# Performance work log

Hardware: AMD Instinct MI355X
Metric: run time of the kernel (lower is better)

Reference implementation:

```python
import jax, jax.numpy as jnp
import numpy as np

B, L, D = 4, 2048, 256
EXPAND, D_STATE, D_CONV = 2, 16, 4
D_INNER = EXPAND * D
DT_RANK = (D + 15) // 16  # ceil(d_model/16) = 16
N_HEADS = 4
H_MLP = int(D * 4.0)
EPS = 1e-5


def _ln(x, w, b):
    mu = x.mean(-1, keepdims=True)
    var = ((x - mu) ** 2).mean(-1, keepdims=True)
    return (x - mu) / jnp.sqrt(var + EPS) * w + b


def _silu(x):
    return x * jax.nn.sigmoid(x)


def _mamba(x, Win, convw, convb, Wx, Wdt, bdt, Alog, Dp, Wout):
    # x: (B, L, D) -> (B, L, D). Standard Mamba mixer (selective scan).
    b, l, d = x.shape
    xz = x @ Win.T                      # (b, l, 2*d_inner)
    xi, z = jnp.split(xz, 2, axis=-1)
    # depthwise causal conv1d, kernel D_CONV
    xc = jnp.swapaxes(xi, 1, 2)         # (b, d_inner, l)
    xc = jax.lax.conv_general_dilated(
        xc, convw, (1,), [(D_CONV - 1, 0)],
        feature_group_count=D_INNER, dimension_numbers=('NCW', 'OIW', 'NCW'))
    xi = _silu(jnp.swapaxes(xc + convb[None, :, None], 1, 2))  # (b, l, d_inner)
    dbl = xi @ Wx.T                     # (b, l, dt_rank + 2*d_state)
    dt = jax.nn.softplus(dbl[..., :DT_RANK] @ Wdt.T + bdt)     # (b, l, d_inner)
    Bm = dbl[..., DT_RANK:DT_RANK + D_STATE]                    # (b, l, n)
    Cm = dbl[..., DT_RANK + D_STATE:]                            # (b, l, n)
    A = -jnp.exp(Alog)                  # (d_inner, n)

    def step(h, ins):
        dt_t, B_t, C_t, u_t = ins       # (b,d_inner),(b,n),(b,n),(b,d_inner)
        h = h * jnp.exp(dt_t[..., None] * A) + dt_t[..., None] * B_t[:, None, :] * u_t[..., None]
        return h, jnp.einsum('bdn,bn->bd', h, C_t)

    xs = tuple(jnp.swapaxes(t, 0, 1) for t in (dt, Bm, Cm, xi))  # time-major
    h0 = jnp.zeros((b, D_INNER, D_STATE), x.dtype)
    _, ys = jax.lax.scan(step, h0, xs)  # ys: (l, b, d_inner)
    y = jnp.swapaxes(ys, 0, 1) + xi * Dp
    return (y * _silu(z)) @ Wout.T


def _attn(x, Wqkv, bqkv, Wo, bo):
    b, l, d = x.shape
    hd = d // N_HEADS
    qkv = x @ Wqkv.T + bqkv
    q, k, v = jnp.split(qkv, 3, axis=-1)
    sh = lambda t: t.reshape(b, l, N_HEADS, hd).transpose(0, 2, 1, 3)
    q, k, v = sh(q), sh(k), sh(v)
    a = jax.nn.softmax(jnp.einsum('bhqd,bhkd->bhqk', q, k) / np.float32(np.sqrt(hd)), axis=-1)
    o = jnp.einsum('bhqk,bhkd->bhqd', a, v).transpose(0, 2, 1, 3).reshape(b, l, d)
    return o @ Wo.T + bo


def setup_inputs() -> dict:
    key = jax.random.key(0)
    ks = iter(jax.random.split(key, 40))
    rn = lambda shape, s=0.02: jax.random.normal(next(ks), shape, jnp.float32) * s
    inp = {'x': jax.random.normal(next(ks), (B, L, D), jnp.float32)}
    for p in ('mf', 'mb'):
        inp[p + '_Win'] = rn((2 * D_INNER, D))
        inp[p + '_convw'] = rn((D_INNER, 1, D_CONV), 0.1)
        inp[p + '_convb'] = jnp.zeros((D_INNER,), jnp.float32)
        inp[p + '_Wx'] = rn((DT_RANK + 2 * D_STATE, D_INNER))
        inp[p + '_Wdt'] = rn((D_INNER, DT_RANK), 0.1)
        inp[p + '_bdt'] = rn((D_INNER,), 0.5)
        inp[p + '_Alog'] = jnp.log(jnp.broadcast_to(jnp.arange(1, D_STATE + 1, dtype=jnp.float32), (D_INNER, D_STATE)))
        inp[p + '_D'] = jnp.ones((D_INNER,), jnp.float32)
        inp[p + '_Wout'] = rn((D, D_INNER))
    for n in ('n1', 'n2', 'n3'):
        inp[n + 'w'] = jnp.ones((D,), jnp.float32)
        inp[n + 'b'] = jnp.zeros((D,), jnp.float32)
    inp['Wqkv'] = rn((3 * D, D))
    inp['bqkv'] = jnp.zeros((3 * D,), jnp.float32)
    inp['Wo'] = rn((D, D))
    inp['bo'] = jnp.zeros((D,), jnp.float32)
    inp['fc1w'] = rn((H_MLP, D))
    inp['fc1b'] = jnp.zeros((H_MLP,), jnp.float32)
    inp['fc2w'] = rn((D, H_MLP))
    inp['fc2b'] = jnp.zeros((D,), jnp.float32)
    return inp


def reference(x, n1w, n1b, n2w, n2b, n3w, n3b,
              mf_Win, mf_convw, mf_convb, mf_Wx, mf_Wdt, mf_bdt, mf_Alog, mf_D, mf_Wout,
              mb_Win, mb_convw, mb_convb, mb_Wx, mb_Wdt, mb_bdt, mb_Alog, mb_D, mb_Wout,
              Wqkv, bqkv, Wo, bo, fc1w, fc1b, fc2w, fc2b):
    # Mamba branch (bidirectional): DropPath is identity at eval
    h = _ln(x, n1w, n1b)
    fwd = _mamba(h, mf_Win, mf_convw, mf_convb, mf_Wx, mf_Wdt, mf_bdt, mf_Alog, mf_D, mf_Wout)
    bwd = jnp.flip(_mamba(jnp.flip(h, 1), mb_Win, mb_convw, mb_convb, mb_Wx, mb_Wdt, mb_bdt, mb_Alog, mb_D, mb_Wout), 1)
    x = x + fwd + bwd
    # Attention branch (full attention since window=None)
    x = x + _attn(_ln(x, n2w, n2b), Wqkv, bqkv, Wo, bo)
    # MLP branch (exact GELU like torch default)
    h = _ln(x, n3w, n3b)
    x = x + (jax.nn.gelu(h @ fc1w.T + fc1b, approximate=False) @ fc2w.T + fc2b)
    return x
```

## Files before the change

### kernel.cpp

```cpp
#include <hip/hip_runtime.h>
#include <hip/hip_bf16.h>
#include <math.h>

#define LL 2048
#define DD 256
#define MTOT 8192
#define DINNER 512
#define CT 32
#define NC 64

typedef __attribute__((ext_vector_type(8))) short short8;
typedef __attribute__((ext_vector_type(4))) float f32x4;

__device__ __forceinline__ float us2f(unsigned short u){
  return __uint_as_float(((unsigned)u) << 16);
}
__device__ __forceinline__ unsigned short f2us(float f){
  __hip_bfloat16 h = __float2bfloat16(f);
  return *(unsigned short*)&h;
}
__device__ __forceinline__ float frcp(float x){
  return __builtin_amdgcn_rcpf(x);
}

__global__ void probe_kernel(const unsigned* __restrict__ alog, int* __restrict__ flag){
  if (threadIdx.x == 0 && blockIdx.x == 0) *flag = (alog[0] != 0u) ? 1 : 0;
}

struct Srcs { const void* p[32]; unsigned off[33]; unsigned foff[32]; };

__global__ __launch_bounds__(256) void cvt_all_kernel(Srcs s, float* __restrict__ dst,
                                                      unsigned short* __restrict__ db,
                                                      const int* __restrict__ flag,
                                                      unsigned total){
  unsigned i = blockIdx.x * 256u + threadIdx.x;
  if (i >= total) return;
  int k = 31;
  while (s.off[k] > i) --k;
  unsigned j = i - s.off[k];
  float v;
  if (*flag) v = us2f(((const unsigned short*)s.p[k])[j]);
  else       v = ((const float*)s.p[k])[j];
  if ((k == 24 && j < 65536u) || (k == 25 && j < 256u)) v *= 0.125f;
  db[i] = f2us(v);
  if (s.foff[k] != 0xFFFFFFFFu) dst[s.foff[k] + j] = v;
}

__global__ __launch_bounds__(256) void cvt_x_kernel(const void* __restrict__ src,
                                                    float* __restrict__ dst,
                                                    const int* __restrict__ flag, unsigned n){
  unsigned i = blockIdx.x * 256u + threadIdx.x;
  if (i >= n) return;
  if (*flag) dst[i] = us2f(((const unsigned short*)src)[i]);
  else       dst[i] = ((const float*)src)[i];
}

__global__ __launch_bounds__(256) void wdbl_prep_kernel(
    const float* __restrict__ Wx, int dsWx, unsigned short* __restrict__ Wd)
{
  const unsigned g = blockIdx.x * 256u + threadIdx.x;
  const int dir = g >> 15;
  const unsigned idx = g & 32767u;
  const int n = idx >> 9, k = idx & 511;
  float v = (n < 48) ? (Wx + (size_t)dir * dsWx)[(size_t)n * 512 + k] : 0.f;
  Wd[g] = f2us(v);
}

__global__ __launch_bounds__(256) void final_out_kernel(
    const float* __restrict__ xf, void* __restrict__ out,
    const int* __restrict__ flag, unsigned n)
{
  unsigned i = blockIdx.x * 256u + threadIdx.x;
  if (i >= n) return;
  float v = xf[i];
  if (*flag) ((unsigned short*)out)[i] = f2us(v);
  else       ((float*)out)[i] = v;
}

enum { G_BF16=0, G_GELU=1, G_RESID=2, G_STF=3 };
__global__ __launch_bounds__(256) void gemm_mfma_kernel(
    const unsigned short* __restrict__ A, int lda, int agap,
    const unsigned short* __restrict__ W, const unsigned short* __restrict__ W2,
    int Kw, int nsplit, int ksplit, int msplit,
    const float* __restrict__ bias,
    unsigned short* __restrict__ Cb, float* __restrict__ resid,
    int N, int K, int kslices, int mode)
{
  __shared__ unsigned short sA[64][40];
  __shared__ unsigned short sW[64][40];
  const int tid = threadIdx.x;
  const int w = tid >> 6, lane = tid & 63, quad = lane >> 4, l16 = lane & 15;
  const int m0 = blockIdx.y << 6, n0 = blockIdx.x << 6;
  const int ks = blockIdx.z;
  const int kper = K / kslices;
  const int srow = tid >> 2, skc = (tid & 3) << 3;
  int wr = n0 + srow;
  const unsigned short* Wbase = W;
  if (msplit && m0 >= msplit) Wbase = W2;
  if (nsplit && wr >= nsplit){ Wbase = W2; wr -= nsplit; }
  f32x4 acc[4] = {};
  for (int k0 = ks * kper; k0 < ks * kper + kper; k0 += 32){
    int ac = k0 + skc;
    if (agap && ac >= 512) ac += 512;
    short8 av = *(const short8*)(A + (size_t)(m0 + srow) * lda + ac);
    int kk = k0 + skc;
    const unsigned short* Wp = Wbase;
    if (ksplit && kk >= ksplit){ Wp = W2; kk -= ksplit; }
    short8 wv = *(const short8*)(Wp + (size_t)wr * Kw + kk);
    __syncthreads();
    *(short8*)&sA[srow][skc] = av;
    *(short8*)&sW[srow][skc] = wv;
    __syncthreads();
    short8 af = *(const short8*)&sA[w * 16 + l16][quad << 3];
    #pragma unroll
    for (int ns = 0; ns < 4; ++ns){
      short8 wf = *(const short8*)&sW[ns * 16 + l16][quad << 3];
      acc[ns] = __builtin_amdgcn_mfma_f32_16x16x32_bf16(af, wf, acc[ns], 0, 0, 0);
    }
  }
  #pragma unroll
  for (int ns = 0; ns < 4; ++ns){
    const int n = n0 + ns * 16 + l16;
    const float bv = (bias && ks == 0) ? bias[n] : 0.f;
    #pragma unroll
    for (int r = 0; r < 4; ++r){
      const int m = m0 + w * 16 + quad * 4 + r;
      const size_t off = (size_t)m * N + n;
      float v = acc[ns][r] + bv;
      if (mode == G_BF16) Cb[off] = f2us(v);
      else if (mode == G_GELU) Cb[off] = f2us(0.5f * v * (1.f + erff(v * 0.70710678118f)));
      else if (mode == G_RESID) resid[off] += v;
      else resid[off] = v;
    }
  }
}

__global__ __launch_bounds__(256) void gemm128_kernel(
    const unsigned short* __restrict__ A, int lda,
    const unsigned short* __restrict__ W, const unsigned short* __restrict__ W2,
    int Kw, int nsplit, const float* __restrict__ bias,
    unsigned short* __restrict__ Cb, int N, int K, int mode)
{
  __shared__ unsigned short sA[128][40];
  __shared__ unsigned short sW[128][40];
  const int tid = threadIdx.x;
  const int w = tid >> 6, lane = tid & 63, quad = lane >> 4, l16 = lane & 15;
  const int wm = (w >> 1) << 6, wn = (w & 1) << 6;
  const int m0 = blockIdx.y << 7, n0 = blockIdx.x << 7;
  const int srow = tid >> 2, skc = (tid & 3) << 3;
  const unsigned short* wrp0;
  const unsigned short* wrp1;
  {
    int r0 = n0 + srow, r1 = n0 + srow + 64;
    const unsigned short* b0 = W;
    const unsigned short* b1 = W;
    if (nsplit){
      if (r0 >= nsplit){ b0 = W2; r0 -= nsplit; }
      if (r1 >= nsplit){ b1 = W2; r1 -= nsplit; }
    }
    wrp0 = b0 + (size_t)r0 * Kw;
    wrp1 = b1 + (size_t)r1 * Kw;
  }
  const unsigned short* arp0 = A + (size_t)(m0 + srow) * lda;
  const unsigned short* arp1 = A + (size_t)(m0 + srow + 64) * lda;
  f32x4 acc[4][4] = {};
  for (int k0 = 0; k0 < K; k0 += 32){
    short8 av0 = *(const short8*)(arp0 + k0 + skc);
    short8 av1 = *(const short8*)(arp1 + k0 + skc);
    short8 wv0 = *(const short8*)(wrp0 + k0 + skc);
    short8 wv1 = *(const short8*)(wrp1 + k0 + skc);
    __syncthreads();
    *(short8*)&sA[srow][skc] = av0;
    *(short8*)&sA[srow + 64][skc] = av1;
    *(short8*)&sW[srow][skc] = wv0;
    *(short8*)&sW[srow + 64][skc] = wv1;
    __syncthreads();
    short8 af[4], wf[4];
    #pragma unroll
    for (int i = 0; i < 4; ++i){
      af[i] = *(const short8*)&sA[wm + i * 16 + l16][quad << 3];
      wf[i] = *(const short8*)&sW[wn + i * 16 + l16][quad << 3];
    }
    #pragma unroll
    for (int mi = 0; mi < 4; ++mi)
      #pragma unroll
      for (int ni = 0; ni < 4; ++ni)
        acc[mi][ni] = __builtin_amdgcn_mfma_f32_16x16x32_bf16(af[mi], wf[ni], acc[mi][ni], 0, 0, 0);
  }
  #pragma unroll
  for (int ni = 0; ni < 4; ++ni){
    const int n = n0 + wn + ni * 16 + l16;
    const float bv = bias ? bias[n] : 0.f;
    #pragma unroll
    for (int mi = 0; mi < 4; ++mi){
      #pragma unroll
      for (int r = 0; r < 4; ++r){
        const int m = m0 + wm + mi * 16 + quad * 4 + r;
        float v = acc[mi][ni][r] + bv;
        if (mode == G_GELU) v = 0.5f * v * (1.f + erff(v * 0.70710678118f));
        Cb[(size_t)m * N + n] = f2us(v);
      }
    }
  }
}

__global__ __launch_bounds__(256) void ln_kernel(
    const float* __restrict__ xin,
    const float* __restrict__ w, const float* __restrict__ b,
    unsigned short* __restrict__ hout)
{
  const int row = blockIdx.x, tid = threadIdx.x;
  const size_t off = (size_t)row * DD + tid;
  float v = xin[off];
  float s = v, s2 = v * v;
  #pragma unroll
  for (int o = 32; o; o >>= 1){ s += __shfl_xor(s, o); s2 += __shfl_xor(s2, o); }
  __shared__ float ls[4], ls2[4];
  if ((tid & 63) == 0){ ls[tid >> 6] = s; ls2[tid >> 6] = s2; }
  __syncthreads();
  s  = ls[0] + ls[1] + ls[2] + ls[3];
  s2 = ls2[0] + ls2[1] + ls2[2] + ls2[3];
  const float mu  = s * (1.f / DD);
  const float var = s2 * (1.f / DD) - mu * mu;
  const float inv = rsqrtf(var + 1e-5f);
  hout[off] = f2us((v - mu) * inv * w[tid] + b[tid]);
}

__global__ __launch_bounds__(256) void conv_silu_kernel(
    const unsigned short* __restrict__ xzc, const float* __restrict__ convw0, int dsCw,
    const float* __restrict__ convb0, int dsCb, unsigned short* __restrict__ xi)
{
  const unsigned g = blockIdx.x * 256u + threadIdx.x;
  const int c4 = (g & 127) << 2;
  const int t = (g >> 7) & 2047;
  const int b = (g >> 18) & 3;
  const int dir = g >> 20;
  const float* cw = convw0 + (size_t)dir * dsCw;
  float4 acc = *(const float4*)(convb0 + (size_t)dir * dsCb + c4);
  float wv[4][4];
  #pragma unroll
  for (int j = 0; j < 4; ++j) *(float4*)wv[j] = *(const float4*)(cw + (c4 + j) * 4);
  #pragma unroll
  for (int k = 0; k < 4; ++k){
    const int tt = dir ? (t + (3 - k)) : (t - 3 + k);
    if ((unsigned)tt < 2048u){
      ushort4 x = *(const ushort4*)(xzc + ((size_t)(b * 2048 + tt)) * 2048 + dir * 1024 + c4);
      acc.x = fmaf(wv[0][k], us2f(x.x), acc.x);
      acc.y = fmaf(wv[1][k], us2f(x.y), acc.y);
      acc.z = fmaf(wv[2][k], us2f(x.z), acc.z);
      acc.w = fmaf(wv[3][k], us2f(x.w), acc.w);
    }
  }
  ushort4 o;
  o.x = f2us(acc.x * frcp(1.f + __expf(-acc.x)));
  o.y = f2us(acc.y * frcp(1.f + __expf(-acc.y)));
  o.z = f2us(acc.z * frcp(1.f + __expf(-acc.z)));
  o.w = f2us(acc.w * frcp(1.f + __expf(-acc.w)));
  *(ushort4*)(xi + (size_t)dir * 4194304 + ((size_t)(b * 2048 + t)) * 512 + c4) = o;
}

__global__ __launch_bounds__(256) void scan_part1_kernel(
    const unsigned short* __restrict__ xib, int dsXi,
    const float* __restrict__ dblc,
    const float* __restrict__ Alog, int dsAl,
    const float* __restrict__ Wdt0, int dsWdt,
    const float* __restrict__ bdt0, int dsBdt,
    float* __restrict__ dtsum, int dsDts,
    float* __restrict__ hend, int dsHend)
{
  const int bx = blockIdx.x;
  const int dg = bx & 1, c = (bx >> 1) & (NC - 1), b = (bx >> 7) & 3, dir = bx >> 9;
  const int tid = threadIdx.x;
  const int d = dg * 256 + tid;
  const unsigned short* xi_ = xib + (size_t)dir * dsXi;
  const float* Al_ = Alog + (size_t)dir * dsAl;
  __shared__ float sDB[CT][32];
  __shared__ unsigned short sXI[CT][256];
  {
    const int s = tid >> 3, c4 = (tid & 7) << 2;
    const int t = dir ? (LL - 1 - (c * CT + s)) : (c * CT + s);
    *(float4*)&sDB[s][c4] =
      *(const float4*)(dblc + ((size_t)(dir * 8192 + b * LL + t)) * 64 + c4);
  }
  #pragma unroll
  for (int p = 0; p < 4; ++p){
    const int s = p * 8 + (tid >> 5);
    const int dc = (tid & 31) << 3;
    const int t = dir ? (LL - 1 - (c * CT + s)) : (c * CT + s);
    *(short8*)&sXI[s][dc] =
      *(const short8*)(xi_ + ((size_t)(b * LL + t)) * 512 + dg * 256 + dc);
  }
  float wdt[16];
  {
    const float* wr = Wdt0 + (size_t)dir * dsWdt + (size_t)d * 16;
    #pragma unroll
    for (int q = 0; q < 4; ++q) *(float4*)&wdt[q * 4] = *(const float4*)(wr + q * 4);
  }
  const float bdtd = (bdt0 + (size_t)dir * dsBdt)[d];
  float A[16];
  #pragma unroll
  for (int n = 0; n < 16; ++n) A[n] = -__expf(Al_[d * 16 + n]);
  const float A1 = A[0];
  bool fast = true;
  #pragma unroll
  for (int n = 0; n < 16; ++n)
    fast = fast && (fabsf(A[n] - A1 * (n + 1)) <= 1e-4f * fabsf(A1 * (n + 1)) + 1e-30f);
  __syncthreads();
  float h[16];
  #pragma unroll
  for (int n = 0; n < 16; ++n) h[n] = 0.f;
  float dts = 0.f;
  #pragma unroll 1
  for (int s = 0; s < CT; ++s){
    const float uv = us2f(sXI[s][tid]);
    f32x4 dv[4], Bv[4];
    #pragma unroll
    for (int q = 0; q < 4; ++q) dv[q] = *(const f32x4*)&sDB[s][q * 4];
    #pragma unroll
    for (int q = 0; q < 4; ++q) Bv[q] = *(const f32x4*)&sDB[s][16 + q * 4];
    float p0 = 0.f, p1 = 0.f, p2 = 0.f, p3 = 0.f;
    #pragma unroll
    for (int j = 0; j < 4; ++j){
      p0 = fmaf(dv[0][j], wdt[j],      p0);
      p1 = fmaf(dv[1][j], wdt[4 + j],  p1);
      p2 = fmaf(dv[2][j], wdt[8 + j],  p2);
      p3 = fmaf(dv[3][j], wdt[12 + j], p3);
    }
    const float dtpre = bdtd + ((p0 + p1) + (p2 + p3));
    const float dtv = (dtpre > 20.f) ? dtpre : __logf(1.f + __expf(dtpre));
    const float dtu = dtv * uv;
    dts += dtv;
    if (fast){
      const float e1 = __expf(dtv * A1);
      const float e2 = e1 * e1;
      float eo = e1, ev = e2;
      #pragma unroll
      for (int m = 0; m < 8; ++m){
        h[2 * m]     = fmaf(h[2 * m],     eo, dtu * Bv[(2 * m) >> 2][(2 * m) & 3]);
        h[2 * m + 1] = fmaf(h[2 * m + 1], ev, dtu * Bv[(2 * m + 1) >> 2][(2 * m + 1) & 3]);
        eo *= e2; ev *= e2;
      }
    } else {
      #pragma unroll
      for (int n = 0; n < 16; ++n){
        const float e = __expf(dtv * A[n]);
        h[n] = fmaf(h[n], e, dtu * Bv[n >> 2][n & 3]);
      }
    }
  }
  const size_t base = (size_t)dir * dsHend + ((size_t)((b * NC + c) * 512 + d)) * 16;
  #pragma unroll
  for (int q = 0; q < 4; ++q) *(float4*)&hend[base + q * 4] = *(const float4*)&h[q * 4];
  dtsum[(size_t)dir * dsDts + (size_t)(b * NC + c) * 512 + d] = dts;
}

__global__ __launch_bounds__(256) void scan_combine_kernel(
    const float* __restrict__ dtsum, int dsDts,
    float* __restrict__ hend, int dsHend,
    const float* __restrict__ Alog, int dsAl)
{
  const unsigned g = blockIdx.x * 256u + threadIdx.x;
  const int dir = g >> 15;
  const unsigned gg = g & 32767u;
  const int b = gg >> 13, d = (gg >> 4) & 511, n = gg & 15;
  const float A = -__expf((Alog + (size_t)dir * dsAl)[d * 16 + n]);
  const float* dts_ = dtsum + (size_t)dir * dsDts;
  float* he_ = hend + (size_t)dir * dsHend;
  float h = 0.f;
  for (int c = 0; c < NC; ++c){
    const size_t sb = ((size_t)((b * NC + c) * 512 + d)) * 16 + n;
    const float e = __expf(dts_[(size_t)(b * NC + c) * 512 + d] * A);
    const float he = he_[sb];
    he_[sb] = h;
    h = h * e + he;
  }
}

__global__ __launch_bounds__(256) void scan_part2_kernel(
    const unsigned short* __restrict__ xib, int dsXi,
    const float* __restrict__ dblc,
    const unsigned short* __restrict__ zin,
    unsigned short* __restrict__ yout,
    const float* __restrict__ Alog, int dsAl,
    const float* __restrict__ Wdt0, int dsWdt,
    const float* __restrict__ bdt0, int dsBdt,
    const float* __restrict__ Dp, int dsD,
    const float* __restrict__ hin, int dsHend)
{
  const int bx = blockIdx.x;
  const int dg = bx & 1, c = (bx >> 1) & (NC - 1), b = (bx >> 7) & 3, dir = bx >> 9;
  const int tid = threadIdx.x;
  const int d = dg * 256 + tid;
  const unsigned short* xi_ = xib + (size_t)dir * dsXi;
  const unsigned short* z_ = zin + dir * 1024;
  unsigned short* y_ = yout + dir * 1024;
  const float* Al_ = Alog + (size_t)dir * dsAl;
  __shared__ float sDB[CT][48];
  __shared__ unsigned short sXI[CT][256];
  __shared__ unsigned short sZ[CT][256];
  for (int i4 = tid; i4 < 384; i4 += 256){
    const int s = i4 / 12, cc = (i4 - s * 12) << 2;
    const int t = dir ? (LL - 1 - (c * CT + s)) : (c * CT + s);
    *(float4*)&sDB[s][cc] =
      *(const float4*)(dblc + ((size_t)(dir * 8192 + b * LL + t)) * 64 + cc);
  }
  #pragma unroll
  for (int p = 0; p < 4; ++p){
    const int s = p * 8 + (tid >> 5);
    const int dc = (tid & 31) << 3;
    const int t = dir ? (LL - 1 - (c * CT + s)) : (c * CT + s);
    const size_t row = (size_t)(b * LL + t);
    *(short8*)&sXI[s][dc] = *(const short8*)(xi_ + row * 512 + dg * 256 + dc);
    *(short8*)&sZ[s][dc]  = *(const short8*)(z_ + row * 2048 + dg * 256 + dc);
  }
  float wdt[16];
  {
    const float* wr = Wdt0 + (size_t)dir * dsWdt + (size_t)d * 16;
    #pragma unroll
    for (int q = 0; q < 4; ++q) *(float4*)&wdt[q * 4] = *(const float4*)(wr + q * 4);
  }
  const float bdtd = (bdt0 + (size_t)dir * dsBdt)[d];
  float A[16];
  #pragma unroll
  for (int n = 0; n < 16; ++n) A[n] = -__expf(Al_[d * 16 + n]);
  const float A1 = A[0];
  bool fast = true;
  #pragma unroll
  for (int n = 0; n < 16; ++n)
    fast = fast && (fabsf(A[n] - A1 * (n + 1)) <= 1e-4f * fabsf(A1 * (n + 1)) + 1e-30f);
  const float Dv = (Dp + (size_t)dir * dsD)[d];
  __syncthreads();
  float h[16];
  const size_t base = (size_t)dir * dsHend + ((size_t)((b * NC + c) * 512 + d)) * 16;
  #pragma unroll
  for (int q = 0; q < 4; ++q) *(float4*)&h[q * 4] = *(const float4*)&hin[base + q * 4];
  #pragma unroll 1
  for (int s = 0; s < CT; ++s){
    const int t = dir ? (LL - 1 - (c * CT + s)) : (c * CT + s);
    const size_t row = (size_t)(b * LL + t);
    const float uv = us2f(sXI[s][tid]);
    const float z  = us2f(sZ[s][tid]);
    f32x4 dv[4];
    #pragma unroll
    for (int q = 0; q < 4; ++q) dv[q] = *(const f32x4*)&sDB[s][q * 4];
    float p0 = 0.f, p1 = 0.f, p2 = 0.f, p3 = 0.f;
    #pragma unroll
    for (int j = 0; j < 4; ++j){
      p0 = fmaf(dv[0][j], wdt[j],      p0);
      p1 = fmaf(dv[1][j], wdt[4 + j],  p1);
      p2 = fmaf(dv[2][j], wdt[8 + j],  p2);
      p3 = fmaf(dv[3][j], wdt[12 + j], p3);
    }
    const float dtpre = bdtd + ((p0 + p1) + (p2 + p3));
    const float dtv = (dtpre > 20.f) ? dtpre : __logf(1.f + __expf(dtpre));
    const float dtu = dtv * uv;
    f32x4 Bv[4], Cv[4];
    #pragma unroll
    for (int q = 0; q < 4; ++q) Bv[q] = *(const f32x4*)&sDB[s][16 + q * 4];
    #pragma unroll
    for (int q = 0; q < 4; ++q) Cv[q] = *(const f32x4*)&sDB[s][32 + q * 4];
    float pA = uv * Dv, pB = 0.f;
    if (fast){
      const float e1 = __expf(dtv * A1);
      const float e2 = e1 * e1;
      float eo = e1, ev = e2;
      #pragma unroll
      for (int m = 0; m < 8; ++m){
        const int n0 = 2 * m, n1 = 2 * m + 1;
        h[n0] = fmaf(h[n0], eo, dtu * Bv[n0 >> 2][n0 & 3]);
        pA = fmaf(h[n0], Cv[n0 >> 2][n0 & 3], pA);
        h[n1] = fmaf(h[n1], ev, dtu * Bv[n1 >> 2][n1 & 3]);
        pB = fmaf(h[n1], Cv[n1 >> 2][n1 & 3], pB);
        eo *= e2; ev *= e2;
      }
    } else {
      #pragma unroll
      for (int n = 0; n < 16; ++n){
        const float e = __expf(dtv * A[n]);
        h[n] = fmaf(h[n], e, dtu * Bv[n >> 2][n & 3]);
        pA = fmaf(h[n], Cv[n >> 2][n & 3], pA);
      }
    }
    const float p = pA + pB;
    const float sig = frcp(1.f + __expf(-z));
    y_[row * 2048 + d] = f2us(p * z * sig);
  }
}

__global__ __launch_bounds__(256) void v_prep_kernel(
    const unsigned short* __restrict__ qkvb, unsigned short* __restrict__ Vt)
{
  const int kt = blockIdx.x;
  const int bh = blockIdx.y;
  const int b = bh >> 2, h = bh & 3;
  __shared__ unsigned short tile[64][72];
  #pragma unroll
  for (int rr = 0; rr < 4; ++rr){
    const int idx = (rr * 256 + threadIdx.x) * 4;
    const int key = idx >> 6, d = idx & 63;
    ushort4 v = *(const ushort4*)(qkvb + ((size_t)(b * 2048 + kt * 64 + key)) * 768 + 512 + h * 64 + d);
    *(ushort4*)&tile[key][d] = v;
  }
  __syncthreads();
  #pragma unroll
  for (int rr = 0; rr < 8; ++rr){
    const int o2 = rr * 256 + threadIdx.x;
    const int d = o2 >> 5, k2 = (o2 & 31) << 1;
    ushort2 u;
    u.x = tile[k2][d];
    u.y = tile[k2 + 1][d];
    *(ushort2*)(Vt + (size_t)bh * 131072 + (size_t)d * 2048 + kt * 64 + k2) = u;
  }
}

__global__ __launch_bounds__(256) void attn_mfma_kernel(
    const unsigned short* __restrict__ qkvb, const unsigned short* __restrict__ Vt,
    float* __restrict__ op0, float* __restrict__ op1, float* __restrict__ lpart)
{
  __shared__ unsigned short sK[64][72];
  __shared__ unsigned short sV[64][72];
  __shared__ unsigned short sP[4][32][68];
  const int tid = threadIdx.x;
  const int w = tid >> 6, lane = tid & 63, quad = lane >> 4, l16 = lane & 15;
  const int bh = blockIdx.y;
  const int b = bh >> 2, h = bh & 3;
  const int q0 = blockIdx.x * 128;
  const int split = blockIdx.z;

  short8 qf[2][2];
  #pragma unroll
  for (int qs = 0; qs < 2; ++qs){
    const unsigned short* qp = qkvb + ((size_t)(b * 2048 + q0 + w * 32 + qs * 16 + l16)) * 768 + h * 64 + quad * 8;
    qf[qs][0] = *(const short8*)qp;
    qf[qs][1] = *(const short8*)(qp + 32);
  }

  f32x4 o[2][4] = {};
  float lsum[2][4] = {};

  const int kt0 = split * 512;
  for (int kt = kt0; kt < kt0 + 512; kt += 64){
    __syncthreads();
    #pragma unroll
    for (int r = 0; r < 2; ++r){
      const int idx = (r * 256 + tid) * 8;
      const int row = idx >> 6, c = idx & 63;
      *(short8*)&sK[row][c] = *(const short8*)(qkvb + ((size_t)(b * 2048 + kt + row)) * 768 + 256 + h * 64 + c);
      *(short8*)&sV[row][c] = *(const short8*)(Vt + (size_t)bh * 131072 + (size_t)row * 2048 + kt + c);
    }
    __syncthreads();

    #pragma unroll
    for (int qs = 0; qs < 2; ++qs){
      float p[4][4];
      #pragma unroll
      for (int sub = 0; sub < 4; ++sub){
        short8 bk0 = *(const short8*)&sK[sub * 16 + l16][quad * 8];
        short8 bk1 = *(const short8*)&sK[sub * 16 + l16][32 + quad * 8];
        f32x4 acc = {0,0,0,0};
        acc = __builtin_amdgcn_mfma_f32_16x16x32_bf16(qf[qs][0], bk0, acc, 0, 0, 0);
        acc = __builtin_amdgcn_mfma_f32_16x16x32_bf16(qf[qs][1], bk1, acc, 0, 0, 0);
        #pragma unroll
        for (int r = 0; r < 4; ++r) p[sub][r] = __expf(acc[r]);
      }
      #pragma unroll
      for (int r = 0; r < 4; ++r)
        lsum[qs][r] += p[0][r] + p[1][r] + p[2][r] + p[3][r];
      #pragma unroll
      for (int sub = 0; sub < 4; ++sub)
        #pragma unroll
        for (int r = 0; r < 4; ++r)
          sP[w][qs * 16 + quad * 4 + r][sub * 16 + l16] = f2us(p[sub][r]);
    }
    __builtin_amdgcn_s_waitcnt(0);
    #pragma unroll
    for (int qs = 0; qs < 2; ++qs){
      short8 pa0 = *(const short8*)&sP[w][qs * 16 + l16][quad * 8];
      short8 pa1 = *(const short8*)&sP[w][qs * 16 + l16][32 + quad * 8];
      #pragma unroll
      for (int nsub = 0; nsub < 4; ++nsub){
        short8 bv0 = *(const short8*)&sV[nsub * 16 + l16][quad * 8];
        short8 bv1 = *(const short8*)&sV[nsub * 16 + l16][32 + quad * 8];
        o[qs][nsub] = __builtin_amdgcn_mfma_f32_16x16x32_bf16(pa0, bv0, o[qs][nsub], 0, 0, 0);
        o[qs][nsub] = __builtin_amdgcn_mfma_f32_16x16x32_bf16(pa1, bv1, o[qs][nsub], 0, 0, 0);
      }
    }
  }

  float* op = (split < 2 ? op0 : op1) + (size_t)(split & 1) * 2097152;
  #pragma unroll
  for (int qs = 0; qs < 2; ++qs){
    #pragma unroll
    for (int r = 0; r < 4; ++r){
      float l = lsum[qs][r];
      l += __shfl_xor(l, 1); l += __shfl_xor(l, 2);
      l += __shfl_xor(l, 4); l += __shfl_xor(l, 8);
      const int q = q0 + w * 32 + qs * 16 + quad * 4 + r;
      #pragma unroll
      for (int nsub = 0; nsub < 4; ++nsub)
        op[((size_t)bh * 2048 + q) * 64 + nsub * 16 + l16] = o[qs][nsub][r];
      if (l16 == 0) lpart[(split * 16 + bh) * 2048 + q] = l;
    }
  }
}

__global__ __launch_bounds__(256) void attn_merge_kernel(
    const float* __restrict__ op0, const float* __restrict__ op1,
    const float* __restrict__ lpart, unsigned short* __restrict__ outp)
{
  const unsigned g = blockIdx.x * 256u + threadIdx.x;
  const int d4 = (g & 15) << 2;
  const int q = (g >> 4) & 2047;
  const int bh = g >> 15;
  float4 s = make_float4(0.f, 0.f, 0.f, 0.f);
  float l = 0.f;
  #pragma unroll
  for (int sp = 0; sp < 4; ++sp){
    const float* op = (sp < 2 ? op0 : op1) + (size_t)(sp & 1) * 2097152;
    float4 o = *(const float4*)(op + ((size_t)bh * 2048 + q) * 64 + d4);
    s.x += o.x; s.y += o.y; s.z += o.z; s.w += o.w;
    l += lpart[(sp * 16 + bh) * 2048 + q];
  }
  const float invl = 1.f / l;
  const int b = bh >> 2, h = bh & 3;
  ushort4 u;
  u.x = f2us(s.x * invl);
  u.y = f2us(s.y * invl);
  u.z = f2us(s.z * invl);
  u.w = f2us(s.w * invl);
  *(ushort4*)(outp + ((size_t)(b * 2048 + q)) * 256 + h * 64 + d4) = u;
}

extern "C" void kernel_launch(void* const* d_in, const int* in_sizes, int n_in,
                              void* d_out, int out_size, void* d_ws, size_t ws_size,
                              hipStream_t stream)
{
  static const bool needf[33] = {
    false, false,true,true,true,true,true,true,true,false,
    false,true,true,true,true,true,true,true,false,
    true,true,true,true,true,true,
    false,true,false,true,false,true,false,true };

  int* flag  = (int*)d_ws;
  float* wts = (float*)d_ws + 16;

  Srcs srcs;
  unsigned acc = 0, facc = 0;
  unsigned foff_h[33];
  for (int i = 1; i <= 32; ++i){
    srcs.p[i - 1] = d_in[i];
    srcs.off[i - 1] = acc;
    acc += (unsigned)in_sizes[i];
    if (needf[i]){ srcs.foff[i - 1] = facc; foff_h[i] = facc; facc += (unsigned)in_sizes[i]; }
    else { srcs.foff[i - 1] = 0xFFFFFFFFu; foff_h[i] = 0xFFFFFFFFu; }
  }
  srcs.off[32] = acc;
  const unsigned wtotal = acc;
  const unsigned ftot = (facc + 3u) & ~3u;

  unsigned short* wb16 = (unsigned short*)(wts + ftot);
  float* xf    = wts + ftot + (wtotal + 1) / 2;
  float* xzc_f = xf + 2097152;
  float* xi_f  = xzc_f + 8388608;
  float* dblc  = xi_f + 4194304;
  float* hb_f  = dblc + 1048576;
  float* hend  = hb_f + 1048576;
  float* dtsum = hend + 4194304;
  float* wd_f  = dtsum + 262144;

  unsigned short* xzc  = (unsigned short*)xzc_f;
  unsigned short* xi16 = (unsigned short*)xi_f;
  unsigned short* hb16 = (unsigned short*)hb_f;
  unsigned short* wdbl = (unsigned short*)wd_f;
  unsigned short* qkvb = xzc;
  unsigned short* Vt   = (unsigned short*)hend;
  float* op0   = xzc_f + 4194304;
  float* op1   = xi_f;
  float* lpart = dtsum;
  unsigned short* fc1o = xzc;

  auto wp  = [&](int i){ return wts + foff_h[i]; };
  auto wp16= [&](int i){ return wb16 + srcs.off[i - 1]; };

  hipLaunchKernelGGL(probe_kernel, dim3(1), dim3(64), 0, stream,
      (const unsigned*)d_in[7], flag);
  hipLaunchKernelGGL(cvt_all_kernel, dim3((wtotal + 255) / 256), dim3(256), 0, stream,
      srcs, wts, wb16, flag, wtotal);
  hipLaunchKernelGGL(cvt_x_kernel, dim3(MTOT * DD / 256), dim3(256), 0, stream,
      d_in[0], xf, flag, (unsigned)(MTOT * DD));

  const int dsCw = (int)(foff_h[11] - foff_h[2]);
  const int dsAl = (int)(foff_h[16] - foff_h[7]);
  const int dsD  = (int)(foff_h[17] - foff_h[8]);
  const int dsWx = (int)(foff_h[13] - foff_h[4]);
  const int dsWdt= (int)(foff_h[14] - foff_h[5]);
  const int dsBdt= (int)(foff_h[15] - foff_h[6]);
  const int dsCb2= (int)(foff_h[12] - foff_h[3]);

  hipLaunchKernelGGL(wdbl_prep_kernel, dim3(256), dim3(256), 0, stream,
      wp(4), dsWx, wdbl);

  auto gemm16 = [&](const unsigned short* Ab, int lda, int agap, int M,
                    const unsigned short* W, const unsigned short* W2,
                    int Kw, int nsplit, int ksplit, int msplit, const float* bias,
                    unsigned short* Cb, float* resid,
                    int N, int K, int ksl, int mode){
    hipLaunchKernelGGL(gemm_mfma_kernel, dim3(N / 64, M / 64, ksl), dim3(256), 0, stream,
        Ab, lda, agap, W, W2, Kw, nsplit, ksplit, msplit, bias, Cb, resid, N, K, ksl, mode);
  };
  auto gemm128 = [&](const unsigned short* Ab, int lda, int M,
                     const unsigned short* W, const unsigned short* W2,
                     int Kw, int nsplit, const float* bias,
                     unsigned short* Cb, int N, int K, int mode){
    hipLaunchKernelGGL(gemm128_kernel, dim3(N / 128, M / 128), dim3(256), 0, stream,
        Ab, lda, W, W2, Kw, nsplit, bias, Cb, N, K, mode);
  };

  hipLaunchKernelGGL(ln_kernel, dim3(MTOT), dim3(256), 0, stream,
      xf, wp(19), wp(20), hb16);

  gemm128(hb16, 256, MTOT, wp16(1), wp16(10), 256, 1024, nullptr,
          xzc, 2048, 256, G_BF16);
  hipLaunchKernelGGL(conv_silu_kernel, dim3(8192), dim3(256), 0, stream,
      xzc, wp(2), dsCw, wp(3), dsCb2, xi16);
  gemm16(xi16, 512, 0, 2 * MTOT, wdbl, wdbl + 32768, 512, 0, 0, MTOT, nullptr,
         nullptr, dblc, 64, 512, 1, G_STF);
  hipLaunchKernelGGL(scan_part1_kernel, dim3(1024), dim3(256), 0, stream,
      xi16, 4194304, dblc, wp(7), dsAl, wp(5), dsWdt, wp(6), dsBdt,
      dtsum, 131072, hend, 2097152);
  hipLaunchKernelGGL(scan_combine_kernel, dim3(256), dim3(256), 0, stream,
      dtsum, 131072, hend, 2097152, wp(7), dsAl);
  hipLaunchKernelGGL(scan_part2_kernel, dim3(1024), dim3(256), 0, stream,
      xi16, 4194304, dblc, xzc + 512, xzc, wp(7), dsAl, wp(5), dsWdt, wp(6), dsBdt,
      wp(8), dsD, hend, 2097152);
  gemm16(xzc, 2048, 1, MTOT, wp16(9), wp16(18), 512, 0, 512, 0, nullptr,
         nullptr, xf, 256, 1024, 1, G_RESID);

  hipLaunchKernelGGL(ln_kernel, dim3(MTOT), dim3(256), 0, stream,
      xf, wp(21), wp(22), hb16);
  gemm128(hb16, 256, MTOT, wp16(25), nullptr, 256, 0, wp(26),
          qkvb, 768, 256, G_BF16);
  hipLaunchKernelGGL(v_prep_kernel, dim3(32, 16), dim3(256), 0, stream,
      qkvb, Vt);
  hipLaunchKernelGGL(attn_mfma_kernel, dim3(16, 16, 4), dim3(256), 0, stream,
      qkvb, Vt, op0, op1, lpart);
  hipLaunchKernelGGL(attn_merge_kernel, dim3(2048), dim3(256), 0, stream,
      op0, op1, lpart, hb16);
  gemm16(hb16, 256, 0, MTOT, wp16(27), nullptr, 256, 0, 0, 0, wp(28),
         nullptr, xf, 256, 256, 1, G_RESID);

  hipLaunchKernelGGL(ln_kernel, dim3(MTOT), dim3(256), 0, stream,
      xf, wp(23), wp(24), hb16);
  gemm128(hb16, 256, MTOT, wp16(29), nullptr, 256, 0, wp(30),
          fc1o, 1024, 256, G_GELU);
  gemm16(fc1o, 1024, 0, MTOT, wp16(31), nullptr, 1024, 0, 0, 0, nullptr,
         nullptr, xf, 256, 1024, 1, G_RESID);
  hipLaunchKernelGGL(final_out_kernel, dim3(MTOT * DD / 256), dim3(256), 0, stream,
      xf, d_out, flag, (unsigned)(MTOT * DD));
}
```

Measured before the change: 439.9 us.

## Fuse input/output conversion, parallelize scan combine, drop attention split-K merge

Folds the input dtype conversion into the first layernorm and the final output conversion into the last GEMM epilogue, removing two elementwise kernels. Replaces the serial per-chunk scan combine loop with a wavefront-parallel prefix scan over chunks using shuffles, launched with many more blocks. Restructures attention to process 64 queries per block over the full key range, normalizing in-kernel, which removes the split-K partial buffers and the merge kernel at the cost of fewer, longer-running blocks.

```diff
diff --git a/kernel.cpp b/kernel.cpp
--- a/kernel.cpp
+++ b/kernel.cpp
@@ -46,15 +46,6 @@
   if (s.foff[k] != 0xFFFFFFFFu) dst[s.foff[k] + j] = v;
 }
 
-__global__ __launch_bounds__(256) void cvt_x_kernel(const void* __restrict__ src,
-                                                    float* __restrict__ dst,
-                                                    const int* __restrict__ flag, unsigned n){
-  unsigned i = blockIdx.x * 256u + threadIdx.x;
-  if (i >= n) return;
-  if (*flag) dst[i] = us2f(((const unsigned short*)src)[i]);
-  else       dst[i] = ((const float*)src)[i];
-}
-
 __global__ __launch_bounds__(256) void wdbl_prep_kernel(
     const float* __restrict__ Wx, int dsWx, unsigned short* __restrict__ Wd)
 {
@@ -66,25 +57,15 @@
   Wd[g] = f2us(v);
 }
 
-__global__ __launch_bounds__(256) void final_out_kernel(
-    const float* __restrict__ xf, void* __restrict__ out,
-    const int* __restrict__ flag, unsigned n)
-{
-  unsigned i = blockIdx.x * 256u + threadIdx.x;
-  if (i >= n) return;
-  float v = xf[i];
-  if (*flag) ((unsigned short*)out)[i] = f2us(v);
-  else       ((float*)out)[i] = v;
-}
-
-enum { G_BF16=0, G_GELU=1, G_RESID=2, G_STF=3 };
+enum { G_BF16=0, G_GELU=1, G_RESID=2, G_STF=3, G_OUT=4 };
 __global__ __launch_bounds__(256) void gemm_mfma_kernel(
     const unsigned short* __restrict__ A, int lda, int agap,
     const unsigned short* __restrict__ W, const unsigned short* __restrict__ W2,
     int Kw, int nsplit, int ksplit, int msplit,
     const float* __restrict__ bias,
     unsigned short* __restrict__ Cb, float* __restrict__ resid,
-    int N, int K, int kslices, int mode)
+    int N, int K, int kslices, int mode,
+    const int* __restrict__ flag, void* __restrict__ outp)
 {
   __shared__ unsigned short sA[64][40];
   __shared__ unsigned short sW[64][40];
@@ -94,6 +75,7 @@
   const int ks = blockIdx.z;
   const int kper = K / kslices;
   const int srow = tid >> 2, skc = (tid & 3) << 3;
+  const int fl = flag ? *flag : 0;
   int wr = n0 + srow;
   const unsigned short* Wbase = W;
   if (msplit && m0 >= msplit) Wbase = W2;
@@ -130,7 +112,12 @@
       if (mode == G_BF16) Cb[off] = f2us(v);
       else if (mode == G_GELU) Cb[off] = f2us(0.5f * v * (1.f + erff(v * 0.70710678118f)));
       else if (mode == G_RESID) resid[off] += v;
-      else resid[off] = v;
+      else if (mode == G_STF) resid[off] = v;
+      else {
+        const float t = v + resid[off];
+        if (fl) ((unsigned short*)outp)[off] = f2us(t);
+        else    ((float*)outp)[off] = t;
+      }
     }
   }
 }
@@ -212,6 +199,32 @@
   const int row = blockIdx.x, tid = threadIdx.x;
   const size_t off = (size_t)row * DD + tid;
   float v = xin[off];
+  float s = v, s2 = v * v;
+  #pragma unroll
+  for (int o = 32; o; o >>= 1){ s += __shfl_xor(s, o); s2 += __shfl_xor(s2, o); }
+  __shared__ float ls[4], ls2[4];
+  if ((tid & 63) == 0){ ls[tid >> 6] = s; ls2[tid >> 6] = s2; }
+  __syncthreads();
+  s  = ls[0] + ls[1] + ls[2] + ls[3];
+  s2 = ls2[0] + ls2[1] + ls2[2] + ls2[3];
+  const float mu  = s * (1.f / DD);
+  const float var = s2 * (1.f / DD) - mu * mu;
+  const float inv = rsqrtf(var + 1e-5f);
+  hout[off] = f2us((v - mu) * inv * w[tid] + b[tid]);
+}
+
+__global__ __launch_bounds__(256) void ln_first_kernel(
+    const void* __restrict__ src, const int* __restrict__ flag,
+    float* __restrict__ xf,
+    const float* __restrict__ w, const float* __restrict__ b,
+    unsigned short* __restrict__ hout)
+{
+  const int row = blockIdx.x, tid = threadIdx.x;
+  const size_t off = (size_t)row * DD + tid;
+  float v;
+  if (*flag) v = us2f(((const unsigned short*)src)[off]);
+  else       v = ((const float*)src)[off];
+  xf[off] = v;
   float s = v, s2 = v * v;
   #pragma unroll
   for (int o = 32; o; o >>= 1){ s += __shfl_xor(s, o); s2 += __shfl_xor(s2, o); }
@@ -359,21 +372,26 @@
     float* __restrict__ hend, int dsHend,
     const float* __restrict__ Alog, int dsAl)
 {
-  const unsigned g = blockIdx.x * 256u + threadIdx.x;
-  const int dir = g >> 15;
-  const unsigned gg = g & 32767u;
-  const int b = gg >> 13, d = (gg >> 4) & 511, n = gg & 15;
+  const int tid = threadIdx.x;
+  const int lane = tid & 63;
+  const unsigned gw = blockIdx.x * 4u + (tid >> 6);
+  const int n = gw & 15, d = (gw >> 4) & 511, b = (gw >> 13) & 3, dir = gw >> 15;
   const float A = -__expf((Alog + (size_t)dir * dsAl)[d * 16 + n]);
   const float* dts_ = dtsum + (size_t)dir * dsDts;
   float* he_ = hend + (size_t)dir * dsHend;
-  float h = 0.f;
-  for (int c = 0; c < NC; ++c){
-    const size_t sb = ((size_t)((b * NC + c) * 512 + d)) * 16 + n;
-    const float e = __expf(dts_[(size_t)(b * NC + c) * 512 + d] * A);
-    const float he = he_[sb];
-    he_[sb] = h;
-    h = h * e + he;
-  }
+  const int c = lane;
+  const size_t sb = ((size_t)((b * NC + c) * 512 + d)) * 16 + n;
+  float E = __expf(dts_[(size_t)(b * NC + c) * 512 + d] * A);
+  float H = he_[sb];
+  #pragma unroll
+  for (int off = 1; off < 64; off <<= 1){
+    const float Eu = __shfl_up(E, off);
+    const float Hu = __shfl_up(H, off);
+    if (lane >= off){ H = fmaf(Hu, E, H); E = Eu * E; }
+  }
+  float hin = __shfl_up(H, 1);
+  if (lane == 0) hin = 0.f;
+  he_[sb] = hin;
 }
 
 __global__ __launch_bounds__(256) void scan_part2_kernel(
@@ -515,31 +533,28 @@
 
 __global__ __launch_bounds__(256) void attn_mfma_kernel(
     const unsigned short* __restrict__ qkvb, const unsigned short* __restrict__ Vt,
-    float* __restrict__ op0, float* __restrict__ op1, float* __restrict__ lpart)
+    unsigned short* __restrict__ outp)
 {
   __shared__ unsigned short sK[64][72];
   __shared__ unsigned short sV[64][72];
-  __shared__ unsigned short sP[4][32][68];
+  __shared__ unsigned short sP[4][16][68];
   const int tid = threadIdx.x;
   const int w = tid >> 6, lane = tid & 63, quad = lane >> 4, l16 = lane & 15;
   const int bh = blockIdx.y;
   const int b = bh >> 2, h = bh & 3;
-  const int q0 = blockIdx.x * 128;
-  const int split = blockIdx.z;
-
-  short8 qf[2][2];
-  #pragma unroll
-  for (int qs = 0; qs < 2; ++qs){
-    const unsigned short* qp = qkvb + ((size_t)(b * 2048 + q0 + w * 32 + qs * 16 + l16)) * 768 + h * 64 + quad * 8;
-    qf[qs][0] = *(const short8*)qp;
-    qf[qs][1] = *(const short8*)(qp + 32);
-  }
-
-  f32x4 o[2][4] = {};
-  float lsum[2][4] = {};
-
-  const int kt0 = split * 512;
-  for (int kt = kt0; kt < kt0 + 512; kt += 64){
+  const int q0 = blockIdx.x * 64;
+
+  short8 qf[2];
+  {
+    const unsigned short* qp = qkvb + ((size_t)(b * 2048 + q0 + w * 16 + l16)) * 768 + h * 64 + quad * 8;
+    qf[0] = *(const short8*)qp;
+    qf[1] = *(const short8*)(qp + 32);
+  }
+
+  f32x4 o[4] = {};
+  float lsum[4] = {};
+
+  for (int kt = 0; kt < 2048; kt += 64){
     __syncthreads();
     #pragma unroll
     for (int r = 0; r < 2; ++r){
@@ -550,85 +565,49 @@
     }
     __syncthreads();
 
-    #pragma unroll
-    for (int qs = 0; qs < 2; ++qs){
-      float p[4][4];
+    float p[4][4];
+    #pragma unroll
+    for (int sub = 0; sub < 4; ++sub){
+      short8 bk0 = *(const short8*)&sK[sub * 16 + l16][quad * 8];
+      short8 bk1 = *(const short8*)&sK[sub * 16 + l16][32 + quad * 8];
+      f32x4 acc = {0,0,0,0};
+      acc = __builtin_amdgcn_mfma_f32_16x16x32_bf16(qf[0], bk0, acc, 0, 0, 0);
+      acc = __builtin_amdgcn_mfma_f32_16x16x32_bf16(qf[1], bk1, acc, 0, 0, 0);
       #pragma unroll
-      for (int sub = 0; sub < 4; ++sub){
-        short8 bk0 = *(const short8*)&sK[sub * 16 + l16][quad * 8];
-        short8 bk1 = *(const short8*)&sK[sub * 16 + l16][32 + quad * 8];
-        f32x4 acc = {0,0,0,0};
-        acc = __builtin_amdgcn_mfma_f32_16x16x32_bf16(qf[qs][0], bk0, acc, 0, 0, 0);
-        acc = __builtin_amdgcn_mfma_f32_16x16x32_bf16(qf[qs][1], bk1, acc, 0, 0, 0);
-        #pragma unroll
-        for (int r = 0; r < 4; ++r) p[sub][r] = __expf(acc[r]);
-      }
+      for (int r = 0; r < 4; ++r) p[sub][r] = __expf(acc[r]);
+    }
+    #pragma unroll
+    for (int r = 0; r < 4; ++r)
+      lsum[r] += p[0][r] + p[1][r] + p[2][r] + p[3][r];
+    #pragma unroll
+    for (int sub = 0; sub < 4; ++sub)
       #pragma unroll
       for (int r = 0; r < 4; ++r)
-        lsum[qs][r] += p[0][r] + p[1][r] + p[2][r] + p[3][r];
-      #pragma unroll
-      for (int sub = 0; sub < 4; ++sub)
-        #pragma unroll
-        for (int r = 0; r < 4; ++r)
-          sP[w][qs * 16 + quad * 4 + r][sub * 16 + l16] = f2us(p[sub][r]);
-    }
+        sP[w][quad * 4 + r][sub * 16 + l16] = f2us(p[sub][r]);
     __builtin_amdgcn_s_waitcnt(0);
-    #pragma unroll
-    for (int qs = 0; qs < 2; ++qs){
-      short8 pa0 = *(const short8*)&sP[w][qs * 16 + l16][quad * 8];
-      short8 pa1 = *(const short8*)&sP[w][qs * 16 + l16][32 + quad * 8];
-      #pragma unroll
-      for (int nsub = 0; nsub < 4; ++nsub){
-        short8 bv0 = *(const short8*)&sV[nsub * 16 + l16][quad * 8];
-        short8 bv1 = *(const short8*)&sV[nsub * 16 + l16][32 + quad * 8];
-        o[qs][nsub] = __builtin_amdgcn_mfma_f32_16x16x32_bf16(pa0, bv0, o[qs][nsub], 0, 0, 0);
-        o[qs][nsub] = __builtin_amdgcn_mfma_f32_16x16x32_bf16(pa1, bv1, o[qs][nsub], 0, 0, 0);
-      }
-    }
-  }
-
-  float* op = (split < 2 ? op0 : op1) + (size_t)(split & 1) * 2097152;
-  #pragma unroll
-  for (int qs = 0; qs < 2; ++qs){
-    #pragma unroll
-    for (int r = 0; r < 4; ++r){
-      float l = lsum[qs][r];
-      l += __shfl_xor(l, 1); l += __shfl_xor(l, 2);
-      l += __shfl_xor(l, 4); l += __shfl_xor(l, 8);
-      const int q = q0 + w * 32 + qs * 16 + quad * 4 + r;
-      #pragma unroll
-      for (int nsub = 0; nsub < 4; ++nsub)
-        op[((size_t)bh * 2048 + q) * 64 + nsub * 16 + l16] = o[qs][nsub][r];
-      if (l16 == 0) lpart[(split * 16 + bh) * 2048 + q] = l;
-    }
-  }
-}
-
-__global__ __launch_bounds__(256) void attn_merge_kernel(
-    const float* __restrict__ op0, const float* __restrict__ op1,
-    const float* __restrict__ lpart, unsigned short* __restrict__ outp)
-{
-  const unsigned g = blockIdx.x * 256u + threadIdx.x;
-  const int d4 = (g & 15) << 2;
-  const int q = (g >> 4) & 2047;
-  const int bh = g >> 15;
-  float4 s = make_float4(0.f, 0.f, 0.f, 0.f);
-  float l = 0.f;
-  #pragma unroll
-  for (int sp = 0; sp < 4; ++sp){
-    const float* op = (sp < 2 ? op0 : op1) + (size_t)(sp & 1) * 2097152;
-    float4 o = *(const float4*)(op + ((size_t)bh * 2048 + q) * 64 + d4);
-    s.x += o.x; s.y += o.y; s.z += o.z; s.w += o.w;
-    l += lpart[(sp * 16 + bh) * 2048 + q];
-  }
-  const float invl = 1.f / l;
-  const int b = bh >> 2, h = bh & 3;
-  ushort4 u;
-  u.x = f2us(s.x * invl);
-  u.y = f2us(s.y * invl);
-  u.z = f2us(s.z * invl);
-  u.w = f2us(s.w * invl);
-  *(ushort4*)(outp + ((size_t)(b * 2048 + q)) * 256 + h * 64 + d4) = u;
+    short8 pa0 = *(const short8*)&sP[w][l16][quad * 8];
+    short8 pa1 = *(const short8*)&sP[w][l16][32 + quad * 8];
+    #pragma unroll
+    for (int nsub = 0; nsub < 4; ++nsub){
+      short8 bv0 = *(const short8*)&sV[nsub * 16 + l16][quad * 8];
+      short8 bv1 = *(const short8*)&sV[nsub * 16 + l16][32 + quad * 8];
+      o[nsub] = __builtin_amdgcn_mfma_f32_16x16x32_bf16(pa0, bv0, o[nsub], 0, 0, 0);
+      o[nsub] = __builtin_amdgcn_mfma_f32_16x16x32_bf16(pa1, bv1, o[nsub], 0, 0, 0);
+    }
+  }
+
+  #pragma unroll
+  for (int r = 0; r < 4; ++r){
+    float l = lsum[r];
+    l += __shfl_xor(l, 1); l += __shfl_xor(l, 2);
+    l += __shfl_xor(l, 4); l += __shfl_xor(l, 8);
+    const float invl = frcp(l);
+    const int q = q0 + w * 16 + quad * 4 + r;
+    #pragma unroll
+    for (int nsub = 0; nsub < 4; ++nsub)
+      outp[((size_t)(b * 2048 + q)) * 256 + h * 64 + nsub * 16 + l16] =
+          f2us(o[nsub][r] * invl);
+  }
 }
 
 extern "C" void kernel_launch(void* const* d_in, const int* in_sizes, int n_in,
@@ -674,9 +653,6 @@
   unsigned short* wdbl = (unsigned short*)wd_f;
   unsigned short* qkvb = xzc;
   unsigned short* Vt   = (unsigned short*)hend;
-  float* op0   = xzc_f + 4194304;
-  float* op1   = xi_f;
-  float* lpart = dtsum;
   unsigned short* fc1o = xzc;
 
   auto wp  = [&](int i){ return wts + foff_h[i]; };
@@ -686,8 +662,6 @@
       (const unsigned*)d_in[7], flag);
   hipLaunchKernelGGL(cvt_all_kernel, dim3((wtotal + 255) / 256), dim3(256), 0, stream,
       srcs, wts, wb16, flag, wtotal);
-  hipLaunchKernelGGL(cvt_x_kernel, dim3(MTOT * DD / 256), dim3(256), 0, stream,
-      d_in[0], xf, flag, (unsigned)(MTOT * DD));
 
   const int dsCw = (int)(foff_h[11] - foff_h[2]);
   const int dsAl = (int)(foff_h[16] - foff_h[7]);
@@ -704,9 +678,10 @@
                     const unsigned short* W, const unsigned short* W2,
                     int Kw, int nsplit, int ksplit, int msplit, const float* bias,
                     unsigned short* Cb, float* resid,
-                    int N, int K, int ksl, int mode){
+                    int N, int K, int ksl, int mode, void* outp = nullptr){
     hipLaunchKernelGGL(gemm_mfma_kernel, dim3(N / 64, M / 64, ksl), dim3(256), 0, stream,
-        Ab, lda, agap, W, W2, Kw, nsplit, ksplit, msplit, bias, Cb, resid, N, K, ksl, mode);
+        Ab, lda, agap, W, W2, Kw, nsplit, ksplit, msplit, bias, Cb, resid, N, K, ksl, mode,
+        (const int*)flag, outp);
   };
   auto gemm128 = [&](const unsigned short* Ab, int lda, int M,
                      const unsigned short* W, const unsigned short* W2,
@@ -716,8 +691,8 @@
         Ab, lda, W, W2, Kw, nsplit, bias, Cb, N, K, mode);
   };
 
-  hipLaunchKernelGGL(ln_kernel, dim3(MTOT), dim3(256), 0, stream,
-      xf, wp(19), wp(20), hb16);
+  hipLaunchKernelGGL(ln_first_kernel, dim3(MTOT), dim3(256), 0, stream,
+      d_in[0], flag, xf, wp(19), wp(20), hb16);
 
   gemm128(hb16, 256, MTOT, wp16(1), wp16(10), 256, 1024, nullptr,
           xzc, 2048, 256, G_BF16);
@@ -728,7 +703,7 @@
   hipLaunchKernelGGL(scan_part1_kernel, dim3(1024), dim3(256), 0, stream,
       xi16, 4194304, dblc, wp(7), dsAl, wp(5), dsWdt, wp(6), dsBdt,
       dtsum, 131072, hend, 2097152);
-  hipLaunchKernelGGL(scan_combine_kernel, dim3(256), dim3(256), 0, stream,
+  hipLaunchKernelGGL(scan_combine_kernel, dim3(16384), dim3(256), 0, stream,
       dtsum, 131072, hend, 2097152, wp(7), dsAl);
   hipLaunchKernelGGL(scan_part2_kernel, dim3(1024), dim3(256), 0, stream,
       xi16, 4194304, dblc, xzc + 512, xzc, wp(7), dsAl, wp(5), dsWdt, wp(6), dsBdt,
@@ -742,10 +717,8 @@
           qkvb, 768, 256, G_BF16);
   hipLaunchKernelGGL(v_prep_kernel, dim3(32, 16), dim3(256), 0, stream,
       qkvb, Vt);
-  hipLaunchKernelGGL(attn_mfma_kernel, dim3(16, 16, 4), dim3(256), 0, stream,
-      qkvb, Vt, op0, op1, lpart);
-  hipLaunchKernelGGL(attn_merge_kernel, dim3(2048), dim3(256), 0, stream,
-      op0, op1, lpart, hb16);
+  hipLaunchKernelGGL(attn_mfma_kernel, dim3(32, 16), dim3(256), 0, stream,
+      qkvb, Vt, hb16);
   gemm16(hb16, 256, 0, MTOT, wp16(27), nullptr, 256, 0, 0, 0, wp(28),
          nullptr, xf, 256, 256, 1, G_RESID);
 
@@ -754,7 +727,5 @@
   gemm128(hb16, 256, MTOT, wp16(29), nullptr, 256, 0, wp(30),
           fc1o, 1024, 256, G_GELU);
   gemm16(fc1o, 1024, 0, MTOT, wp16(31), nullptr, 1024, 0, 0, 0, nullptr,
-         nullptr, xf, 256, 1024, 1, G_RESID);
-  hipLaunchKernelGGL(final_out_kernel, dim3(MTOT * DD / 256), dim3(256), 0, stream,
-      xf, d_out, flag, (unsigned)(MTOT * DD));
-}
+         nullptr, xf, 256, 1024, 1, G_OUT, d_out);
+}
```

Result: slower. 502.3 us (+14.2%).
